# Performance work log

Hardware: AMD Instinct MI355X
Metric: run time of the kernel (lower is better)

Reference implementation:

```python
import jax, jax.numpy as jnp
import numpy as np

N = 262144   # 512x512 flattened grid points
U = 256      # RBF units


def setup_inputs() -> dict:
    key = jax.random.key(0)
    ks = jax.random.split(key, 10)
    inp = {
        "x": jax.random.uniform(ks[0], (N, 1), dtype=jnp.float32),
        "y": jax.random.uniform(ks[1], (N, 1), dtype=jnp.float32),
        "u": jax.random.normal(ks[2], (N, 1), dtype=jnp.float32),
        "v": jax.random.normal(ks[3], (N, 1), dtype=jnp.float32),
        "diff_u": jax.random.normal(ks[4], (N, 1), dtype=jnp.float32),
        "diff_v": jax.random.normal(ks[5], (N, 1), dtype=jnp.float32),
        # RBF layer params: mu [2, U] uniform in [0, max_val=1], beta init = 1/sigma2 = 0.5
        "mu_u": jax.random.uniform(ks[6], (2, U), dtype=jnp.float32),
        "beta_u": jnp.full((U,), 0.5, dtype=jnp.float32),
        "W_u": jax.random.normal(ks[7], (U, 1), dtype=jnp.float32) * 0.1,
        "mu_v": jax.random.uniform(ks[8], (2, U), dtype=jnp.float32),
        "beta_v": jnp.full((U,), 0.5, dtype=jnp.float32),
        "W_v": jax.random.normal(ks[9], (U, 1), dtype=jnp.float32) * 0.1,
        # PDE scalar variables (values from __init__)
        "d_var": jnp.array([60.0], dtype=jnp.float32),
        "a_var": jnp.array([12.0], dtype=jnp.float32),
        "b_var": jnp.array([15.0], dtype=jnp.float32),
        "u_mean_var": jnp.array([0.9068], dtype=jnp.float32),
        "v_mean_var": jnp.array([0.38], dtype=jnp.float32),
        "u_scale_var": jnp.array([2.5], dtype=jnp.float32),
        "v_scale_var": jnp.array([0.1], dtype=jnp.float32),
    }
    return inp


def _rbf_net(x, y, mu, beta, W):
    """Gaussian-RBF + Dense(1, no bias). Returns (pred [N,1], laplacian [N,1]).

    The Laplacian is the closed form of the nested tape.gradient in the
    original TF code: for phi = exp(-beta*r2) with r2 = (x-mux)^2 + (y-muy)^2,
    d2phi/dx2 + d2phi/dy2 = phi * (4*beta^2*r2 - 4*beta).
    """
    dxm = x - mu[0]                      # [N, U]
    dym = y - mu[1]                      # [N, U]
    r2 = dxm * dxm + dym * dym           # [N, U]
    phi = jnp.exp(-beta * r2)            # [N, U]
    pred = phi @ W                       # [N, 1]
    lap = (phi * (4.0 * beta * beta * r2 - 4.0 * beta)) @ W  # [N, 1]
    return pred, lap


# loss weights (self.weight_* in the original; set to 1.0 here)
W_PDE_U = 1.0
W_DIFF_U = 1.0
W_PDE_V = 1.0
W_DIFF_V = 1.0


def reference(x, y, u, v, diff_u, diff_v,
              mu_u, beta_u, W_u, mu_v, beta_v, W_v,
              d_var, a_var, b_var, u_mean_var, v_mean_var,
              u_scale_var, v_scale_var):
    u_pred, lap_u = _rbf_net(x, y, mu_u, beta_u, W_u)
    v_pred, lap_v = _rbf_net(x, y, mu_v, beta_v, W_v)

    loss_u = jnp.mean(jnp.square(u_pred - u))
    loss_v = jnp.mean(jnp.square(v_pred - v))

    u_phys = u_pred * u_scale_var + u_mean_var   # [N,1]
    v_phys = v_pred * v_scale_var + v_mean_var   # [N,1]
    denom = 1.0 + u_phys * u_phys                # [N,1]

    loss_pde_u = jnp.mean(jnp.square(
        d_var * lap_u + a_var / u_scale_var - u_pred - u_mean_var / u_scale_var
        - b_var * (4.0 * (u_pred + u_mean_var / u_scale_var) * v_phys) / denom))
    loss_diff_u = jnp.mean(jnp.square(lap_u - diff_u))

    loss_pde_v = jnp.mean(jnp.square(
        lap_v + u_phys / v_scale_var
        - b_var * u_phys * (v_pred + v_mean_var / v_scale_var) / denom))
    loss_diff_v = jnp.mean(jnp.square(lap_v - diff_v))

    # main branch of _get_losses2 (iterations % 100 != 0)
    loss1 = (0.1 * loss_u + 0.1 * loss_v
             + W_PDE_U * loss_pde_u + W_DIFF_U * loss_diff_u
             + W_PDE_V * loss_pde_v + W_DIFF_V * loss_diff_v)

    return (loss1, loss_u, loss_pde_u, loss_v, loss_pde_v, loss_diff_u, loss_diff_v)
```

## Files before the change

### kernel.cpp

```cpp
#include <hip/hip_runtime.h>
#include <hip/hip_bf16.h>
#include <math.h>

#define NPTS   262144
#define UNITS  256
#define STR    15
#define NCO    225
#define LSTR   16
#define OFF_PU 0
#define OFF_LU 208
#define OFF_PV 448
#define OFF_LV 656
#define CFTOT  896
#define PBLK   64
#define PPT    4
#define MTPB   256
#define MBLK   256
#define QSTRIDE 65536

__device__ __constant__ float CC[8] = {
    0.99985117f, -0.99903214f, 0.49728235f, -0.16237637f,
    0.03751734f, -0.00582524f, 0.00046232f, 0.0f };

__global__ __launch_bounds__(256) void rbf_prep(
    const float* __restrict__ mu_u, const float* __restrict__ beta_u,
    const float* __restrict__ W_u,
    const float* __restrict__ mu_v, const float* __restrict__ beta_v,
    const float* __restrict__ W_v,
    float* __restrict__ partial, int* __restrict__ flagBlk)
{
    const int tid  = threadIdx.x;
    const int bid  = blockIdx.x;
    const int w    = tid >> 6;
    const int lane = tid & 63;
    const int j    = bid * 4 + w;

    __shared__ float pwA[4][NCO];
    __shared__ float pwB[4][NCO];
    __shared__ int   sflag[4];

    int cidx[4], gi[4], gm[4];
    #pragma unroll
    for (int r = 0; r < 4; ++r) {
        const int c = lane + 64 * r;
        cidx[r] = c;
        gi[r]   = c / STR;
        gm[r]   = c - STR * gi[r];
    }

    float accPu[4] = {0,0,0,0}, accLu[4] = {0,0,0,0};
    float accPv[4] = {0,0,0,0}, accLv[4] = {0,0,0,0};
    int badAll = 0;

    #pragma unroll
    for (int s = 0; s < 2; ++s) {
        const float* mu = s ? mu_v   : mu_u;
        const float* be = s ? beta_v : beta_u;
        const float* W  = s ? W_v    : W_u;
        const float mx  = mu[j], my = mu[UNITS + j];
        const float b   = be[j], wgt = W[j];

        const float xlo = -0.05f, xhi = 1.05f;
        const float dxl = xlo - mx, dxh = xhi - mx;
        const float dyl = xlo - my, dyh = xhi - my;
        const float dx2max = fmaxf(dxl*dxl, dxh*dxh);
        const float dy2max = fmaxf(dyl*dyl, dyh*dyh);
        const float dx2min = (dxl <= 0.f && dxh >= 0.f) ? 0.f : fminf(dxl*dxl, dxh*dxh);
        const float dy2min = (dyl <= 0.f && dyh >= 0.f) ? 0.f : fminf(dyl*dyl, dyh*dyh);
        const float t1 = b * (dx2min + dy2min);
        const float t2 = b * (dx2max + dy2max);
        const float tlo = fminf(t1, t2), thi = fmaxf(t1, t2);
        badAll |= !(thi <= 2.4f && tlo >= -0.2f);

        const float ax = mx - 0.5f, ay = my - 0.5f;
        const float qXX = b, qYY = b;
        const float qX = -2.f*b*ax, qY = -2.f*b*ay;
        const float q0 = b*(ax*ax + ay*ay);

        const float fourwb = 4.f * wgt * b;
        float cP[8], cL[8];
        #pragma unroll
        for (int m = 0; m < 8; ++m) {
            cP[m] = wgt * CC[m];
            cL[m] = fourwb * ((m ? CC[m-1] : 0.f) - CC[m]);
        }

        float* A = &pwA[w][0];
        float* B = &pwB[w][0];
        #pragma unroll
        for (int r = 0; r < 4; ++r) {
            const int c = cidx[r];
            if (c < NCO) {
                float v = 0.f;
                if (c == 0)          v = q0;
                else if (c == 1)     v = qY;
                else if (c == 2)     v = qYY;
                else if (c == STR)   v = qX;
                else if (c == 2*STR) v = qXX;
                A[c] = v;
            }
        }
        __threadfence_block();

        float aP[4] = {0,0,0,0}, aL[4] = {0,0,0,0};
        #pragma unroll
        for (int r = 0; r < 4; ++r)
            if (cidx[r] == 0) { aP[r] = cP[0]; aL[r] = cL[0]; }

        #pragma unroll
        for (int m = 1; m <= 7; ++m) {
            #pragma unroll
            for (int r = 0; r < 4; ++r) {
                const int c = cidx[r];
                if (c < NCO) {
                    const float p = A[c];
                    aP[r] = fmaf(cP[m], p, aP[r]);
                    aL[r] = fmaf(cL[m], p, aL[r]);
                }
            }
            if (m < 7) {
                #pragma unroll
                for (int r = 0; r < 4; ++r) {
                    const int c = cidx[r];
                    if (c < NCO) {
                        float acc = q0 * A[c];
                        if (gm[r] >= 1) acc = fmaf(qY,  A[c-1],     acc);
                        if (gm[r] >= 2) acc = fmaf(qYY, A[c-2],     acc);
                        if (gi[r] >= 1) acc = fmaf(qX,  A[c-STR],   acc);
                        if (gi[r] >= 2) acc = fmaf(qXX, A[c-2*STR], acc);
                        B[c] = acc;
                    }
                }
                float* T = A; A = B; B = T;
                __threadfence_block();
            }
        }
        #pragma unroll
        for (int r = 0; r < 4; ++r) {
            if (s == 0) { accPu[r] = aP[r]; accLu[r] = aL[r]; }
            else        { accPv[r] = aP[r]; accLv[r] = aL[r]; }
        }
        __threadfence_block();
    }
    if (lane == 0) sflag[w] = badAll;

    __syncthreads();
    #pragma unroll
    for (int r = 0; r < 4; ++r) {
        const int c = cidx[r];
        if (c < NCO) { pwA[w][c] = accPu[r]; pwB[w][c] = accLu[r]; }
    }
    __syncthreads();
    if (tid < 448) {
        float v = 0.f;
        if (tid < 208) {
            const int i = tid >> 4, m = tid & 15;
            if (m < 15) {
                const int c = i*STR + m;
                v = pwA[0][c] + pwA[1][c] + pwA[2][c] + pwA[3][c];
            }
        } else {
            const int idx = tid - 208;
            const int i = idx >> 4, m = idx & 15;
            if (m < 15) {
                const int c = i*STR + m;
                v = pwB[0][c] + pwB[1][c] + pwB[2][c] + pwB[3][c];
            }
        }
        partial[bid * CFTOT + tid] = v;
    }
    __syncthreads();
    #pragma unroll
    for (int r = 0; r < 4; ++r) {
        const int c = cidx[r];
        if (c < NCO) { pwA[w][c] = accPv[r]; pwB[w][c] = accLv[r]; }
    }
    __syncthreads();
    if (tid < 448) {
        float v = 0.f;
        if (tid < 208) {
            const int i = tid >> 4, m = tid & 15;
            if (m < 15) {
                const int c = i*STR + m;
                v = pwA[0][c] + pwA[1][c] + pwA[2][c] + pwA[3][c];
            }
        } else {
            const int idx = tid - 208;
            const int i = idx >> 4, m = idx & 15;
            if (m < 15) {
                const int c = i*STR + m;
                v = pwB[0][c] + pwB[1][c] + pwB[2][c] + pwB[3][c];
            }
        }
        partial[bid * CFTOT + 448 + tid] = v;
    }
    if (tid == 0)
        flagBlk[bid] = sflag[0] | sflag[1] | sflag[2] | sflag[3];
}

__global__ __launch_bounds__(256) void rbf_fold(
    const float* __restrict__ partial, const int* __restrict__ flagBlk,
    float* __restrict__ coefF, int* __restrict__ flagAll)
{
    const int tid = threadIdx.x;
    const int c   = blockIdx.x * 256 + tid;
    if (c < CFTOT) {
        float s = 0.f;
        #pragma unroll 8
        for (int p = 0; p < PBLK; ++p)
            s += partial[p * CFTOT + c];
        coefF[c] = s;
    }
    if (blockIdx.x == 0 && tid < 64) {
        int f = flagBlk[tid];
        for (int off = 32; off > 0; off >>= 1)
            f |= __shfl_down(f, off);
        if (tid == 0) *flagAll = f;
    }
}

template<int D>
__device__ __forceinline__ void eval4(const float* sco,
    float X0, float X1, float X2, float X3,
    float Y0, float Y1, float Y2, float Y3,
    float& h0, float& h1, float& h2, float& h3)
{
    h0 = h1 = h2 = h3 = 0.f;
    #pragma unroll
    for (int ii = 0; ii <= D; ++ii) {
        const int i = D - ii;
        const int K = (D - i + 4) / 4;
        float r0 = 0.f, r1 = 0.f, r2 = 0.f, r3 = 0.f;
        #pragma unroll
        for (int kk = 0; kk < K; ++kk) {
            const int k = K - 1 - kk;
            const float4 q = *(const float4*)(sco + i*LSTR + 4*k);
            r0 = fmaf(r0, Y0, q.w); r1 = fmaf(r1, Y1, q.w);
            r2 = fmaf(r2, Y2, q.w); r3 = fmaf(r3, Y3, q.w);
            r0 = fmaf(r0, Y0, q.z); r1 = fmaf(r1, Y1, q.z);
            r2 = fmaf(r2, Y2, q.z); r3 = fmaf(r3, Y3, q.z);
            r0 = fmaf(r0, Y0, q.y); r1 = fmaf(r1, Y1, q.y);
            r2 = fmaf(r2, Y2, q.y); r3 = fmaf(r3, Y3, q.y);
            r0 = fmaf(r0, Y0, q.x); r1 = fmaf(r1, Y1, q.x);
            r2 = fmaf(r2, Y2, q.x); r3 = fmaf(r3, Y3, q.x);
        }
        h0 = fmaf(h0, X0, r0); h1 = fmaf(h1, X1, r1);
        h2 = fmaf(h2, X2, r2); h3 = fmaf(h3, X3, r3);
    }
}

__global__ __launch_bounds__(MTPB) void rbf_main(
    const float* __restrict__ gx, const float* __restrict__ gy,
    const float* __restrict__ gu, const float* __restrict__ gv,
    const float* __restrict__ gdu, const float* __restrict__ gdv,
    const float* __restrict__ coefF, const int* __restrict__ flagAll,
    const float* __restrict__ mu_u, const float* __restrict__ beta_u,
    const float* __restrict__ W_u,
    const float* __restrict__ mu_v, const float* __restrict__ beta_v,
    const float* __restrict__ W_v,
    const float* __restrict__ p_d, const float* __restrict__ p_a,
    const float* __restrict__ p_b, const float* __restrict__ p_um,
    const float* __restrict__ p_vm, const float* __restrict__ p_us,
    const float* __restrict__ p_vs,
    float* __restrict__ part)
{
    const int tid = threadIdx.x;
    const int bid = blockIdx.x;
    const int i0  = bid * MTPB + tid;

    __shared__ __align__(16) float sco[CFTOT];
    if (tid < CFTOT/4)
        ((float4*)sco)[tid] = ((const float4*)coefF)[tid];
    __syncthreads();

    float xs[PPT], ys[PPT];
    #pragma unroll
    for (int p = 0; p < PPT; ++p) {
        xs[p] = gx[i0 + p*QSTRIDE];
        ys[p] = gy[i0 + p*QSTRIDE];
    }

    const int bad = __builtin_amdgcn_readfirstlane(*flagAll);
    bool in = true;
    #pragma unroll
    for (int p = 0; p < PPT; ++p)
        in = in && (xs[p] >= -0.05f) && (xs[p] <= 1.05f)
                && (ys[p] >= -0.05f) && (ys[p] <= 1.05f);
    const bool allIn = __all(in);

    float up[PPT], vp[PPT], lu[PPT], lv[PPT];
    if (!bad && allIn) {
        const float X0 = xs[0]-0.5f, X1 = xs[1]-0.5f, X2 = xs[2]-0.5f, X3 = xs[3]-0.5f;
        const float Y0 = ys[0]-0.5f, Y1 = ys[1]-0.5f, Y2 = ys[2]-0.5f, Y3 = ys[3]-0.5f;
        eval4<12>(sco + OFF_PU, X0,X1,X2,X3, Y0,Y1,Y2,Y3, up[0],up[1],up[2],up[3]);
        eval4<14>(sco + OFF_LU, X0,X1,X2,X3, Y0,Y1,Y2,Y3, lu[0],lu[1],lu[2],lu[3]);
        eval4<12>(sco + OFF_PV, X0,X1,X2,X3, Y0,Y1,Y2,Y3, vp[0],vp[1],vp[2],vp[3]);
        eval4<14>(sco + OFF_LV, X0,X1,X2,X3, Y0,Y1,Y2,Y3, lv[0],lv[1],lv[2],lv[3]);
    } else {
        #pragma unroll
        for (int p = 0; p < PPT; ++p) { up[p]=lu[p]=vp[p]=lv[p]=0.f; }
        for (int jj = 0; jj < UNITS; ++jj) {
            const float mxu = mu_u[jj], myu = mu_u[UNITS + jj];
            const float bu_ = beta_u[jj], wu_ = W_u[jj];
            const float mxv = mu_v[jj], myv = mu_v[UNITS + jj];
            const float bv_ = beta_v[jj], wv_ = W_v[jj];
            #pragma unroll
            for (int p = 0; p < PPT; ++p) {
                {
                    const float dx = xs[p] - mxu, dy = ys[p] - myu;
                    const float r2 = fmaf(dx, dx, dy * dy);
                    const float ph = expf(-bu_ * r2);
                    up[p] = fmaf(wu_, ph, up[p]);
                    lu[p] = fmaf(wu_ * ph, fmaf(4.f*bu_*bu_, r2, -4.f*bu_), lu[p]);
                }
                {
                    const float dx = xs[p] - mxv, dy = ys[p] - myv;
                    const float r2 = fmaf(dx, dx, dy * dy);
                    const float ph = expf(-bv_ * r2);
                    vp[p] = fmaf(wv_, ph, vp[p]);
                    lv[p] = fmaf(wv_ * ph, fmaf(4.f*bv_*bv_, r2, -4.f*bv_), lv[p]);
                }
            }
        }
    }

    const float dd = p_d[0],  aa = p_a[0], bb = p_b[0];
    const float um = p_um[0], vm = p_vm[0];
    const float us = p_us[0], vs = p_vs[0];
    const float iu  = 1.0f / us, iv = 1.0f / vs;
    const float cau = (aa - um) * iu;
    const float c4b = 4.0f * bb * iu;
    const float cbv = bb * iv;

    float s0 = 0.f, s1 = 0.f, s2 = 0.f, s3 = 0.f, s4 = 0.f, s5 = 0.f;
    #pragma unroll
    for (int p = 0; p < PPT; ++p) {
        const int ii = i0 + p*QSTRIDE;
        const float uu  = gu[ii],  vv  = gv[ii];
        const float ddu = gdu[ii], ddv = gdv[ii];
        float eu = up[p] - uu; s0 += eu * eu;
        float ev = vp[p] - vv; s1 += ev * ev;
        float uph = fmaf(up[p], us, um);
        float vph = fmaf(vp[p], vs, vm);
        float den = fmaf(uph, uph, 1.0f);
        float uvd = uph * vph / den;
        float rpu = fmaf(dd, lu[p], cau) - up[p] - c4b * uvd;
        s2 += rpu * rpu;
        float rdu = lu[p] - ddu; s3 += rdu * rdu;
        float rpv = fmaf(uph, iv, lv[p]) - cbv * uvd;
        s4 += rpv * rpv;
        float rdv = lv[p] - ddv; s5 += rdv * rdv;
    }

    float s[6] = { s0, s1, s2, s3, s4, s5 };
    __shared__ float red[4][6];
    #pragma unroll
    for (int k = 0; k < 6; ++k) {
        float vsum = s[k];
        for (int off = 32; off > 0; off >>= 1)
            vsum += __shfl_down(vsum, off);
        s[k] = vsum;
    }
    const int lane = tid & 63;
    const int wid  = tid >> 6;
    if (lane == 0) {
        #pragma unroll
        for (int k = 0; k < 6; ++k) red[wid][k] = s[k];
    }
    __syncthreads();
    if (tid < 6) {
        float p = red[0][tid] + red[1][tid] + red[2][tid] + red[3][tid];
        part[tid * MBLK + bid] = p;
    }
}

__global__ __launch_bounds__(256) void rbf_final(
    const float* __restrict__ part, float* __restrict__ out)
{
    const int tid = threadIdx.x;
    __shared__ float red[4][6];
    float s[6];
    #pragma unroll
    for (int k = 0; k < 6; ++k) {
        float vsum = part[k * MBLK + tid];
        for (int off = 32; off > 0; off >>= 1)
            vsum += __shfl_down(vsum, off);
        s[k] = vsum;
    }
    const int lane = tid & 63;
    const int wid  = tid >> 6;
    if (lane == 0) {
        #pragma unroll
        for (int k = 0; k < 6; ++k) red[wid][k] = s[k];
    }
    __syncthreads();
    if (tid == 0) {
        const float inv = 1.0f / (float)NPTS;
        const float Lu  = (red[0][0] + red[1][0] + red[2][0] + red[3][0]) * inv;
        const float Lv  = (red[0][1] + red[1][1] + red[2][1] + red[3][1]) * inv;
        const float Lpu = (red[0][2] + red[1][2] + red[2][2] + red[3][2]) * inv;
        const float Ldu = (red[0][3] + red[1][3] + red[2][3] + red[3][3]) * inv;
        const float Lpv = (red[0][4] + red[1][4] + red[2][4] + red[3][4]) * inv;
        const float Ldv = (red[0][5] + red[1][5] + red[2][5] + red[3][5]) * inv;
        out[0] = 0.1f * Lu + 0.1f * Lv + Lpu + Ldu + Lpv + Ldv;
        out[1] = Lu;
        out[2] = Lpu;
        out[3] = Lv;
        out[4] = Lpv;
        out[5] = Ldu;
        out[6] = Ldv;
    }
}

extern "C" void kernel_launch(void* const* d_in, const int* in_sizes, int n_in,
                              void* d_out, int out_size, void* d_ws, size_t ws_size,
                              hipStream_t stream) {
    const float* gx   = (const float*)d_in[0];
    const float* gy   = (const float*)d_in[1];
    const float* gu   = (const float*)d_in[2];
    const float* gv   = (const float*)d_in[3];
    const float* gdu  = (const float*)d_in[4];
    const float* gdv  = (const float*)d_in[5];
    const float* mu_u = (const float*)d_in[6];
    const float* be_u = (const float*)d_in[7];
    const float* W_u  = (const float*)d_in[8];
    const float* mu_v = (const float*)d_in[9];
    const float* be_v = (const float*)d_in[10];
    const float* W_v  = (const float*)d_in[11];
    const float* p_d  = (const float*)d_in[12];
    const float* p_a  = (const float*)d_in[13];
    const float* p_b  = (const float*)d_in[14];
    const float* p_um = (const float*)d_in[15];
    const float* p_vm = (const float*)d_in[16];
    const float* p_us = (const float*)d_in[17];
    const float* p_vs = (const float*)d_in[18];

    float* wsf     = (float*)d_ws;
    float* partial = wsf;
    float* coefF   = wsf + 57344;
    float* part    = wsf + 58240;
    int*   flagBlk = (int*)(wsf + 59776);
    int*   flagAll = (int*)(wsf + 59840);
    float* out     = (float*)d_out;

    rbf_prep<<<PBLK, 256, 0, stream>>>(mu_u, be_u, W_u, mu_v, be_v, W_v,
                                       partial, flagBlk);
    rbf_fold<<<4, 256, 0, stream>>>(partial, flagBlk, coefF, flagAll);
    rbf_main<<<MBLK, MTPB, 0, stream>>>(gx, gy, gu, gv, gdu, gdv,
                                        coefF, flagAll,
                                        mu_u, be_u, W_u, mu_v, be_v, W_v,
                                        p_d, p_a, p_b, p_um, p_vm, p_us, p_vs,
                                        part);
    rbf_final<<<1, 256, 0, stream>>>(part, out);
}
```

Baseline: 27.66 us.

## Split RBF prep work per network across twice as many blocks

Each wave in the coefficient-prep kernel previously computed the polynomial expansion for one unit of both networks, one after the other. Now each wave handles a single (unit, network) pair, and the prep grid doubles from 64 to 128 blocks, halving the serial dependency chain per wave. The per-block partial layout is rebuilt so each block writes both nets' sums, and the workspace offsets are shifted to fit the larger buffer. The cost is that the fold kernel reads twice as many partials and now reduces flags with a barrier inside a conditional branch.

```diff
diff --git a/kernel.cpp b/kernel.cpp
--- a/kernel.cpp
+++ b/kernel.cpp
@@ -12,7 +12,7 @@
 #define OFF_PV 448
 #define OFF_LV 656
 #define CFTOT  896
-#define PBLK   64
+#define PBLK   128
 #define PPT    4
 #define MTPB   256
 #define MBLK   256
@@ -33,7 +33,9 @@
     const int bid  = blockIdx.x;
     const int w    = tid >> 6;
     const int lane = tid & 63;
-    const int j    = bid * 4 + w;
+    const int id   = bid * 4 + w;
+    const int j    = id >> 1;
+    const int net  = id & 1;
 
     __shared__ float pwA[4][NCO];
     __shared__ float pwB[4][NCO];
@@ -48,151 +50,117 @@
         gm[r]   = c - STR * gi[r];
     }
 
-    float accPu[4] = {0,0,0,0}, accLu[4] = {0,0,0,0};
-    float accPv[4] = {0,0,0,0}, accLv[4] = {0,0,0,0};
-    int badAll = 0;
-
-    #pragma unroll
-    for (int s = 0; s < 2; ++s) {
-        const float* mu = s ? mu_v   : mu_u;
-        const float* be = s ? beta_v : beta_u;
-        const float* W  = s ? W_v    : W_u;
-        const float mx  = mu[j], my = mu[UNITS + j];
-        const float b   = be[j], wgt = W[j];
-
-        const float xlo = -0.05f, xhi = 1.05f;
-        const float dxl = xlo - mx, dxh = xhi - mx;
-        const float dyl = xlo - my, dyh = xhi - my;
-        const float dx2max = fmaxf(dxl*dxl, dxh*dxh);
-        const float dy2max = fmaxf(dyl*dyl, dyh*dyh);
-        const float dx2min = (dxl <= 0.f && dxh >= 0.f) ? 0.f : fminf(dxl*dxl, dxh*dxh);
-        const float dy2min = (dyl <= 0.f && dyh >= 0.f) ? 0.f : fminf(dyl*dyl, dyh*dyh);
-        const float t1 = b * (dx2min + dy2min);
-        const float t2 = b * (dx2max + dy2max);
-        const float tlo = fminf(t1, t2), thi = fmaxf(t1, t2);
-        badAll |= !(thi <= 2.4f && tlo >= -0.2f);
-
-        const float ax = mx - 0.5f, ay = my - 0.5f;
-        const float qXX = b, qYY = b;
-        const float qX = -2.f*b*ax, qY = -2.f*b*ay;
-        const float q0 = b*(ax*ax + ay*ay);
-
-        const float fourwb = 4.f * wgt * b;
-        float cP[8], cL[8];
-        #pragma unroll
-        for (int m = 0; m < 8; ++m) {
-            cP[m] = wgt * CC[m];
-            cL[m] = fourwb * ((m ? CC[m-1] : 0.f) - CC[m]);
-        }
-
-        float* A = &pwA[w][0];
-        float* B = &pwB[w][0];
+    const float* mu = net ? mu_v   : mu_u;
+    const float* be = net ? beta_v : beta_u;
+    const float* W  = net ? W_v    : W_u;
+    const float mx  = mu[j], my = mu[UNITS + j];
+    const float b   = be[j], wgt = W[j];
+
+    const float xlo = -0.05f, xhi = 1.05f;
+    const float dxl = xlo - mx, dxh = xhi - mx;
+    const float dyl = xlo - my, dyh = xhi - my;
+    const float dx2max = fmaxf(dxl*dxl, dxh*dxh);
+    const float dy2max = fmaxf(dyl*dyl, dyh*dyh);
+    const float dx2min = (dxl <= 0.f && dxh >= 0.f) ? 0.f : fminf(dxl*dxl, dxh*dxh);
+    const float dy2min = (dyl <= 0.f && dyh >= 0.f) ? 0.f : fminf(dyl*dyl, dyh*dyh);
+    const float t1 = b * (dx2min + dy2min);
+    const float t2 = b * (dx2max + dy2max);
+    const float tlo = fminf(t1, t2), thi = fmaxf(t1, t2);
+    const int bad = !(thi <= 2.4f && tlo >= -0.2f);
+    if (lane == 0) sflag[w] = bad;
+
+    const float ax = mx - 0.5f, ay = my - 0.5f;
+    const float qXX = b, qYY = b;
+    const float qX = -2.f*b*ax, qY = -2.f*b*ay;
+    const float q0 = b*(ax*ax + ay*ay);
+
+    const float fourwb = 4.f * wgt * b;
+    float cP[8], cL[8];
+    #pragma unroll
+    for (int m = 0; m < 8; ++m) {
+        cP[m] = wgt * CC[m];
+        cL[m] = fourwb * ((m ? CC[m-1] : 0.f) - CC[m]);
+    }
+
+    float* A = &pwA[w][0];
+    float* B = &pwB[w][0];
+    #pragma unroll
+    for (int r = 0; r < 4; ++r) {
+        const int c = cidx[r];
+        if (c < NCO) {
+            float v = 0.f;
+            if (c == 0)          v = q0;
+            else if (c == 1)     v = qY;
+            else if (c == 2)     v = qYY;
+            else if (c == STR)   v = qX;
+            else if (c == 2*STR) v = qXX;
+            A[c] = v;
+        }
+    }
+    __threadfence_block();
+
+    float aP[4] = {0,0,0,0}, aL[4] = {0,0,0,0};
+    #pragma unroll
+    for (int r = 0; r < 4; ++r)
+        if (cidx[r] == 0) { aP[r] = cP[0]; aL[r] = cL[0]; }
+
+    #pragma unroll
+    for (int m = 1; m <= 7; ++m) {
         #pragma unroll
         for (int r = 0; r < 4; ++r) {
             const int c = cidx[r];
             if (c < NCO) {
-                float v = 0.f;
-                if (c == 0)          v = q0;
-                else if (c == 1)     v = qY;
-                else if (c == 2)     v = qYY;
-                else if (c == STR)   v = qX;
-                else if (c == 2*STR) v = qXX;
-                A[c] = v;
+                const float p = A[c];
+                aP[r] = fmaf(cP[m], p, aP[r]);
+                aL[r] = fmaf(cL[m], p, aL[r]);
             }
         }
-        __threadfence_block();
-
-        float aP[4] = {0,0,0,0}, aL[4] = {0,0,0,0};
-        #pragma unroll
-        for (int r = 0; r < 4; ++r)
-            if (cidx[r] == 0) { aP[r] = cP[0]; aL[r] = cL[0]; }
-
-        #pragma unroll
-        for (int m = 1; m <= 7; ++m) {
+        if (m < 7) {
             #pragma unroll
             for (int r = 0; r < 4; ++r) {
                 const int c = cidx[r];
                 if (c < NCO) {
-                    const float p = A[c];
-                    aP[r] = fmaf(cP[m], p, aP[r]);
-                    aL[r] = fmaf(cL[m], p, aL[r]);
+                    float acc = q0 * A[c];
+                    if (gm[r] >= 1) acc = fmaf(qY,  A[c-1],     acc);
+                    if (gm[r] >= 2) acc = fmaf(qYY, A[c-2],     acc);
+                    if (gi[r] >= 1) acc = fmaf(qX,  A[c-STR],   acc);
+                    if (gi[r] >= 2) acc = fmaf(qXX, A[c-2*STR], acc);
+                    B[c] = acc;
                 }
             }
-            if (m < 7) {
-                #pragma unroll
-                for (int r = 0; r < 4; ++r) {
-                    const int c = cidx[r];
-                    if (c < NCO) {
-                        float acc = q0 * A[c];
-                        if (gm[r] >= 1) acc = fmaf(qY,  A[c-1],     acc);
-                        if (gm[r] >= 2) acc = fmaf(qYY, A[c-2],     acc);
-                        if (gi[r] >= 1) acc = fmaf(qX,  A[c-STR],   acc);
-                        if (gi[r] >= 2) acc = fmaf(qXX, A[c-2*STR], acc);
-                        B[c] = acc;
-                    }
-                }
-                float* T = A; A = B; B = T;
-                __threadfence_block();
-            }
-        }
-        #pragma unroll
-        for (int r = 0; r < 4; ++r) {
-            if (s == 0) { accPu[r] = aP[r]; accLu[r] = aL[r]; }
-            else        { accPv[r] = aP[r]; accLv[r] = aL[r]; }
-        }
-        __threadfence_block();
-    }
-    if (lane == 0) sflag[w] = badAll;
+            float* T = A; A = B; B = T;
+            __threadfence_block();
+        }
+    }
 
     __syncthreads();
     #pragma unroll
     for (int r = 0; r < 4; ++r) {
         const int c = cidx[r];
-        if (c < NCO) { pwA[w][c] = accPu[r]; pwB[w][c] = accLu[r]; }
+        if (c < NCO) { pwA[w][c] = aP[r]; pwB[w][c] = aL[r]; }
     }
     __syncthreads();
-    if (tid < 448) {
-        float v = 0.f;
-        if (tid < 208) {
-            const int i = tid >> 4, m = tid & 15;
-            if (m < 15) {
-                const int c = i*STR + m;
-                v = pwA[0][c] + pwA[1][c] + pwA[2][c] + pwA[3][c];
+    {
+        float* dst = partial + bid * CFTOT;
+        #pragma unroll
+        for (int k = 0; k < 4; ++k) {
+            const int c = tid + 256 * k;
+            if (c < CFTOT) {
+                float v = 0.f;
+                int idx, isLap, nsel;
+                if (c < 208)      { idx = c;       isLap = 0; nsel = 0; }
+                else if (c < 448) { idx = c - 208; isLap = 1; nsel = 0; }
+                else if (c < 656) { idx = c - 448; isLap = 0; nsel = 1; }
+                else              { idx = c - 656; isLap = 1; nsel = 1; }
+                const int i = idx >> 4, m = idx & 15;
+                if (m < 15) {
+                    const int cs = i * STR + m;
+                    if (!isLap) v = pwA[nsel][cs] + pwA[2 + nsel][cs];
+                    else        v = pwB[nsel][cs] + pwB[2 + nsel][cs];
+                }
+                dst[c] = v;
             }
-        } else {
-            const int idx = tid - 208;
-            const int i = idx >> 4, m = idx & 15;
-            if (m < 15) {
-                const int c = i*STR + m;
-                v = pwB[0][c] + pwB[1][c] + pwB[2][c] + pwB[3][c];
-            }
-        }
-        partial[bid * CFTOT + tid] = v;
-    }
-    __syncthreads();
-    #pragma unroll
-    for (int r = 0; r < 4; ++r) {
-        const int c = cidx[r];
-        if (c < NCO) { pwA[w][c] = accPv[r]; pwB[w][c] = accLv[r]; }
-    }
-    __syncthreads();
-    if (tid < 448) {
-        float v = 0.f;
-        if (tid < 208) {
-            const int i = tid >> 4, m = tid & 15;
-            if (m < 15) {
-                const int c = i*STR + m;
-                v = pwA[0][c] + pwA[1][c] + pwA[2][c] + pwA[3][c];
-            }
-        } else {
-            const int idx = tid - 208;
-            const int i = idx >> 4, m = idx & 15;
-            if (m < 15) {
-                const int c = i*STR + m;
-                v = pwB[0][c] + pwB[1][c] + pwB[2][c] + pwB[3][c];
-            }
-        }
-        partial[bid * CFTOT + 448 + tid] = v;
+        }
     }
     if (tid == 0)
         flagBlk[bid] = sflag[0] | sflag[1] | sflag[2] | sflag[3];
@@ -211,11 +179,14 @@
             s += partial[p * CFTOT + c];
         coefF[c] = s;
     }
-    if (blockIdx.x == 0 && tid < 64) {
+    if (blockIdx.x == 0 && tid < 128) {
         int f = flagBlk[tid];
         for (int off = 32; off > 0; off >>= 1)
             f |= __shfl_down(f, off);
-        if (tid == 0) *flagAll = f;
+        __shared__ int ff[2];
+        if ((tid & 63) == 0) ff[tid >> 6] = f;
+        __syncthreads();
+        if (tid == 0) *flagAll = ff[0] | ff[1];
     }
 }
 
@@ -437,10 +408,10 @@
 
     float* wsf     = (float*)d_ws;
     float* partial = wsf;
-    float* coefF   = wsf + 57344;
-    float* part    = wsf + 58240;
-    int*   flagBlk = (int*)(wsf + 59776);
-    int*   flagAll = (int*)(wsf + 59840);
+    float* coefF   = wsf + 114688;
+    float* part    = wsf + 115584;
+    int*   flagBlk = (int*)(wsf + 117120);
+    int*   flagAll = (int*)(wsf + 117248);
     float* out     = (float*)d_out;
 
     rbf_prep<<<PBLK, 256, 0, stream>>>(mu_u, be_u, W_u, mu_v, be_v, W_v,
```

New measurement: 26.76 us, median of 2. 3.2% less time.
